# Kernel tuning notes

Hardware: AMD Instinct MI355X
Metric: run time of the kernel (lower is better)

The kernel has to match this reference:

```python
import jax, jax.numpy as jnp
import numpy as np

NH, WS, SS = 8, 7, 3  # num_heads, window_size, shift_size
EPS = 1e-5


def _rel_pos_index(ws):
    coords = np.stack(np.meshgrid(np.arange(ws), np.arange(ws), indexing='ij'))
    coords = coords.reshape(2, -1)                      # [2, L]
    rel = coords[:, :, None] - coords[:, None, :]       # [2, L, L]
    rel = rel.transpose(1, 2, 0) + (ws - 1)
    return rel[..., 0] * (2 * ws - 1) + rel[..., 1]     # [L, L] int


def _attn_mask(H, W, ws, ss):
    # region labels for shifted-window masking (torchvision semantics)
    img = np.zeros((H, W))
    slices = (slice(0, -ws), slice(-ws, -ss), slice(-ss, None))
    cnt = 0
    for hs in slices:
        for wsl in slices:
            img[hs, wsl] = cnt
            cnt += 1
    win = img.reshape(H // ws, ws, W // ws, ws).transpose(0, 2, 1, 3).reshape(-1, ws * ws)
    mask = (win[:, None, :] != win[:, :, None]).astype(np.float32) * (-100.0)
    return mask  # [nWin, L, L]


def _layernorm(x, gamma, beta):
    mu = jnp.mean(x, axis=-1, keepdims=True)
    var = jnp.mean(jnp.square(x - mu), axis=-1, keepdims=True)
    return (x - mu) * jax.lax.rsqrt(var + EPS) * gamma + beta


def _swin_attention(x, qkv_w, qkv_b, proj_w, proj_b, rpb_table):
    B, H, W, C = x.shape
    HD = C // NH
    L = WS * WS
    nH, nW = H // WS, W // WS
    # cyclic shift
    xs = jnp.roll(x, shift=(-SS, -SS), axis=(1, 2))
    # window partition -> [B*nWin, L, C]
    xw = xs.reshape(B, nH, WS, nW, WS, C).transpose(0, 1, 3, 2, 4, 5).reshape(B * nH * nW, L, C)
    qkv = jnp.einsum('nlc,dc->nld', xw, qkv_w) + qkv_b
    qkv = qkv.reshape(-1, L, 3, NH, HD).transpose(2, 0, 3, 1, 4)  # [3, N, h, L, d]
    q, k, v = qkv[0] * (HD ** -0.5), qkv[1], qkv[2]
    attn = jnp.einsum('nhid,nhjd->nhij', q, k)  # [N, h, L, L]
    bias = rpb_table[jnp.asarray(_rel_pos_index(WS))]  # [L, L, h]
    attn = attn + bias.transpose(2, 0, 1)[None]
    mask = jnp.asarray(_attn_mask(H, W, WS, SS))  # [nWin, L, L]
    nwin = nH * nW
    attn = attn.reshape(B, nwin, NH, L, L) + mask[None, :, None]
    attn = jax.nn.softmax(attn.reshape(-1, NH, L, L), axis=-1)
    out = jnp.einsum('nhij,nhjd->nhid', attn, v).transpose(0, 2, 1, 3).reshape(-1, L, C)
    out = jnp.einsum('nlc,dc->nld', out, proj_w) + proj_b
    # reverse windows and shift
    out = out.reshape(B, nH, nW, WS, WS, C).transpose(0, 1, 3, 2, 4, 5).reshape(B, H, W, C)
    return jnp.roll(out, shift=(SS, SS), axis=(1, 2))


def setup_inputs() -> dict:
    key = jax.random.key(0)
    ks = jax.random.split(key, 8)
    B, H, W, C = 32, 56, 56, 256
    F = 4 * C
    s = 0.02
    return {
        'x': jax.random.normal(ks[0], (B, H, W, C), jnp.float32),
        'qkv_w': jax.random.normal(ks[1], (3 * C, C), jnp.float32) * s,
        'qkv_b': jnp.zeros((3 * C,), jnp.float32),
        'proj_w': jax.random.normal(ks[2], (C, C), jnp.float32) * s,
        'proj_b': jnp.zeros((C,), jnp.float32),
        'rpb_table': jax.random.normal(ks[3], ((2 * WS - 1) ** 2, NH), jnp.float32) * s,
        'gamma1': jnp.ones((C,), jnp.float32),
        'beta1': jnp.zeros((C,), jnp.float32),
        'w1': jax.random.normal(ks[4], (C, F), jnp.float32) * s,
        'b1': jax.random.normal(ks[5], (F,), jnp.float32) * 1e-6,
        'w2': jax.random.normal(ks[6], (F, C), jnp.float32) * s,
        'b2': jax.random.normal(ks[7], (C,), jnp.float32) * 1e-6,
        'gamma2': jnp.ones((C,), jnp.float32),
        'beta2': jnp.zeros((C,), jnp.float32),
    }


def reference(x, qkv_w, qkv_b, proj_w, proj_b, rpb_table, gamma1, beta1, w1, b1, w2, b2, gamma2, beta2):
    # post-norm residual block: x + norm1(attn(x)); x + norm2(mlp(x))
    a = _swin_attention(x, qkv_w, qkv_b, proj_w, proj_b, rpb_table)
    x = x + _layernorm(a, gamma1, beta1)
    h = jax.nn.gelu(jnp.einsum('bhwc,cf->bhwf', x, w1) + b1, approximate=False)
    m = jnp.einsum('bhwf,fc->bhwc', h, w2) + b2
    x = x + _layernorm(m, gamma2, beta2)
    return x
```

## Files before the change

kernel.cpp:

```cpp
#include <hip/hip_runtime.h>
#include <hip/hip_bf16.h>


typedef unsigned short ushort_t;
typedef short bf16x8 __attribute__((ext_vector_type(8)));
typedef float f32x4 __attribute__((ext_vector_type(4)));

__device__ __forceinline__ float bf2f(unsigned short u) {
    union { unsigned int i; float f; } x; x.i = ((unsigned int)u) << 16; return x.f;
}
__device__ __forceinline__ unsigned short f2bf(float f) {
    union { float f; unsigned int i; } x; x.f = f;
    unsigned int r = x.i + 0x7fffu + ((x.i >> 16) & 1u);
    return (unsigned short)(r >> 16);
}
__device__ __forceinline__ bf16x8 pack8(float4 a, float4 b) {
    bf16x8 r;
    r[0] = (short)f2bf(a.x); r[1] = (short)f2bf(a.y);
    r[2] = (short)f2bf(a.z); r[3] = (short)f2bf(a.w);
    r[4] = (short)f2bf(b.x); r[5] = (short)f2bf(b.y);
    r[6] = (short)f2bf(b.z); r[7] = (short)f2bf(b.w);
    return r;
}
__device__ __forceinline__ void gl_lds16(const ushort_t* g, ushort_t* l) {
    __builtin_amdgcn_global_load_lds((const __attribute__((address_space(1))) void*)g,
                                     (__attribute__((address_space(3))) void*)l, 16, 0, 0);
}

__device__ __forceinline__ long swin_src_off(int m) {
    int n = m / 49, l = m - n * 49;
    int b = n >> 6, win = n & 63;
    int wh = win >> 3, ww = win & 7;
    int i = l / 7, j = l - i * 7;
    int hs = wh * 7 + i + 3; if (hs >= 56) hs -= 56;
    int ws = ww * 7 + j + 3; if (ws >= 56) ws -= 56;
    return ((long)(b * 56 + hs) * 56 + ws) * 256;
}

__global__ __launch_bounds__(256)
void xgather(const float* __restrict__ x, ushort_t* __restrict__ xg)
{
    int t = blockIdx.x * 256 + threadIdx.x;
    int row = t >> 5, ch = (t & 31) * 8;
    const float* src = x + swin_src_off(row) + ch;
    float4 a = *(const float4*)src, b = *(const float4*)(src + 4);
    *(bf16x8*)(xg + (long)row * 256 + ch) = pack8(a, b);
}

template<int SRCT>
__global__ __launch_bounds__(256)
void convW(const float* __restrict__ src, ushort_t* __restrict__ dst, int N, int kshift)
{
    int idx = blockIdx.x * 256 + threadIdx.x;
    int kk = idx & ((1 << kshift) - 1), nn = idx >> kshift;
    float v = SRCT ? src[(long)kk * N + nn] : src[idx];
    dst[idx] = f2bf(v);
}

template<int ACT>
__global__ __launch_bounds__(256)
void gemm128(const ushort_t* __restrict__ A, const ushort_t* __restrict__ W,
             const float* __restrict__ bias, ushort_t* __restrict__ C,
             int M, int N, int K)
{
    __shared__ ushort_t As[128 * 32];
    __shared__ ushort_t Bs[128 * 32];
    const int t = threadIdx.x, lane = t & 63, wave = t >> 6;
    const int row0 = blockIdx.x * 128, col0 = blockIdx.y * 128;
    const int wm = (wave >> 1) * 64, wn = (wave & 1) * 64;

    const ushort_t* ag0 = A + (long)(row0 + (t >> 2)) * K + (t & 3) * 8;
    const ushort_t* ag1 = A + (long)(row0 + 64 + (t >> 2)) * K + (t & 3) * 8;
    const ushort_t* bg0 = W + (long)(col0 + (t >> 2)) * K + (t & 3) * 8;
    const ushort_t* bg1 = W + (long)(col0 + 64 + (t >> 2)) * K + (t & 3) * 8;
    ushort_t* la0 = &As[t * 8];        ushort_t* la1 = &As[2048 + t * 8];
    ushort_t* lb0 = &Bs[t * 8];        ushort_t* lb1 = &Bs[2048 + t * 8];

    f32x4 acc[4][4] = {};
    for (int k0 = 0; k0 < K; k0 += 32) {
        __syncthreads();
        gl_lds16(ag0 + k0, la0);
        gl_lds16(ag1 + k0, la1);
        gl_lds16(bg0 + k0, lb0);
        gl_lds16(bg1 + k0, lb1);
        __syncthreads();
        bf16x8 af[4], bw[4];
        #pragma unroll
        for (int i = 0; i < 4; i++) {
            af[i] = *(const bf16x8*)&As[(wm + i * 16 + (lane & 15)) * 32 + (lane >> 4) * 8];
            bw[i] = *(const bf16x8*)&Bs[(wn + i * 16 + (lane & 15)) * 32 + (lane >> 4) * 8];
        }
        #pragma unroll
        for (int mi = 0; mi < 4; mi++)
            #pragma unroll
            for (int ni = 0; ni < 4; ni++)
                acc[mi][ni] = __builtin_amdgcn_mfma_f32_16x16x32_bf16(af[mi], bw[ni], acc[mi][ni], 0, 0, 0);
    }
    #pragma unroll
    for (int mi = 0; mi < 4; mi++)
        #pragma unroll
        for (int ni = 0; ni < 4; ni++) {
            const int c = col0 + wn + ni * 16 + (lane & 15);
            const float bv = bias[c];
            #pragma unroll
            for (int r = 0; r < 4; r++) {
                const int rr = row0 + wm + mi * 16 + (lane >> 4) * 4 + r;
                float v = acc[mi][ni][r] + bv;
                if (ACT) v = 0.5f * v * (1.0f + erff(v * 0.70710678118654752f));
                C[(long)rr * N + c] = f2bf(v);
            }
        }
}

__global__ __launch_bounds__(64)
void attn_mfma(const ushort_t* __restrict__ qkv, const float* __restrict__ rpb,
               ushort_t* __restrict__ out)
{
    __shared__ ushort_t v_t[32 * 72];
    __shared__ ushort_t p_lds[64 * 72];
    __shared__ float bias_s[169];

    const int blk = blockIdx.x;
    const int n = blk >> 3, h = blk & 7;
    const int l = threadIdx.x;
    const long wbase = (long)n * 49 * 768 + h * 32;
    const float scale = 0.17677669529663687f;

    {
        int j = min(l, 48);
        const ushort_t* vr = qkv + wbase + (long)j * 768 + 512;
        #pragma unroll
        for (int c = 0; c < 4; c++) {
            bf16x8 vv = *(const bf16x8*)(vr + c * 8);
            #pragma unroll
            for (int e = 0; e < 8; e++) v_t[(c * 8 + e) * 72 + l] = (ushort_t)vv[e];
        }
    }
    for (int idx = l; idx < 169; idx += 64) bias_s[idx] = rpb[idx * 8 + h];
    __syncthreads();

    f32x4 s[4][4] = {};
    {
        bf16x8 aq[4], bk[4];
        #pragma unroll
        for (int mt = 0; mt < 4; mt++) {
            int i = min(mt * 16 + (l & 15), 48);
            aq[mt] = *(const bf16x8*)(qkv + wbase + (long)i * 768 + (l >> 4) * 8);
        }
        #pragma unroll
        for (int nt = 0; nt < 4; nt++) {
            int j = min(nt * 16 + (l & 15), 48);
            bk[nt] = *(const bf16x8*)(qkv + wbase + (long)j * 768 + 256 + (l >> 4) * 8);
        }
        #pragma unroll
        for (int mt = 0; mt < 4; mt++)
            #pragma unroll
            for (int nt = 0; nt < 4; nt++)
                s[mt][nt] = __builtin_amdgcn_mfma_f32_16x16x32_bf16(aq[mt], bk[nt], s[mt][nt], 0, 0, 0);
    }

    const int win = n & 63, wh = win >> 3, ww = win & 7;
    int yj[4], xj[4], regj[4]; bool jv[4];
    #pragma unroll
    for (int nt = 0; nt < 4; nt++) {
        int j = nt * 16 + (l & 15);
        jv[nt] = (j <= 48);
        int jc = min(j, 48);
        yj[nt] = jc / 7; xj[nt] = jc - yj[nt] * 7;
        int hs = wh * 7 + yj[nt], wsx = ww * 7 + xj[nt];
        regj[nt] = (hs < 49 ? 0 : (hs < 53 ? 1 : 2)) * 3 + (wsx < 49 ? 0 : (wsx < 53 ? 1 : 2));
    }
    float rinv[4][4];
    #pragma unroll
    for (int mt = 0; mt < 4; mt++) {
        #pragma unroll
        for (int r = 0; r < 4; r++) {
            int i = mt * 16 + (l >> 4) * 4 + r;
            int ic = min(i, 48);
            int yi = ic / 7, xi = ic - yi * 7;
            int hs = wh * 7 + yi, wsx = ww * 7 + xi;
            int regi = (hs < 49 ? 0 : (hs < 53 ? 1 : 2)) * 3 + (wsx < 49 ? 0 : (wsx < 53 ? 1 : 2));
            float val[4];
            #pragma unroll
            for (int nt = 0; nt < 4; nt++) {
                float v = s[mt][nt][r] * scale + bias_s[(yi - yj[nt] + 6) * 13 + (xi - xj[nt] + 6)];
                if (regi != regj[nt]) v -= 100.f;
                val[nt] = jv[nt] ? v : -1e30f;
            }
            float mx = fmaxf(fmaxf(val[0], val[1]), fmaxf(val[2], val[3]));
            #pragma unroll
            for (int off = 1; off <= 8; off <<= 1) mx = fmaxf(mx, __shfl_xor(mx, off));
            float sum = 0.f;
            #pragma unroll
            for (int nt = 0; nt < 4; nt++) { val[nt] = __expf(val[nt] - mx); sum += val[nt]; }
            #pragma unroll
            for (int off = 1; off <= 8; off <<= 1) sum += __shfl_xor(sum, off);
            rinv[mt][r] = 1.0f / sum;
            #pragma unroll
            for (int nt = 0; nt < 4; nt++)
                p_lds[i * 72 + nt * 16 + (l & 15)] = f2bf(val[nt]);
        }
    }
    __syncthreads();

    f32x4 o[4][2] = {};
    #pragma unroll
    for (int ks = 0; ks < 2; ks++) {
        bf16x8 pa[4], vb[2];
        #pragma unroll
        for (int mt = 0; mt < 4; mt++)
            pa[mt] = *(const bf16x8*)&p_lds[(mt * 16 + (l & 15)) * 72 + ks * 32 + (l >> 4) * 8];
        #pragma unroll
        for (int nt = 0; nt < 2; nt++)
            vb[nt] = *(const bf16x8*)&v_t[(nt * 16 + (l & 15)) * 72 + ks * 32 + (l >> 4) * 8];
        #pragma unroll
        for (int mt = 0; mt < 4; mt++)
            #pragma unroll
            for (int nt = 0; nt < 2; nt++)
                o[mt][nt] = __builtin_amdgcn_mfma_f32_16x16x32_bf16(pa[mt], vb[nt], o[mt][nt], 0, 0, 0);
    }
    #pragma unroll
    for (int mt = 0; mt < 4; mt++)
        #pragma unroll
        for (int r = 0; r < 4; r++) {
            int i = mt * 16 + (l >> 4) * 4 + r;
            if (i < 49) {
                float rs = rinv[mt][r];
                #pragma unroll
                for (int nt = 0; nt < 2; nt++) {
                    int d = nt * 16 + (l & 15);
                    out[((long)n * 49 + i) * 256 + h * 32 + d] = f2bf(o[mt][nt][r] * rs);
                }
            }
        }
}

__global__ __launch_bounds__(256)
void ln1_kernel(const ushort_t* __restrict__ proj, const float* __restrict__ x,
                const float* __restrict__ gamma, const float* __restrict__ beta,
                float* __restrict__ x1f, ushort_t* __restrict__ x1b)
{
    const int wave = threadIdx.x >> 6, lane = threadIdx.x & 63;
    const int p = blockIdx.x * 4 + wave;
    const int b = p / 3136, rem = p - b * 3136;
    const int hh = rem / 56, wc = rem - hh * 56;
    int hs = hh + 53; if (hs >= 56) hs -= 56;
    int ws = wc + 53; if (ws >= 56) ws -= 56;
    const int wh = hs / 7, ii = hs - wh * 7;
    const int wwi = ws / 7, jj = ws - wwi * 7;
    const long srow = (long)(b * 64 + wh * 8 + wwi) * 49 + ii * 7 + jj;
    const int c = lane * 4;

    ushort4 av = *(const ushort4*)(proj + srow * 256 + c);
    float a0 = bf2f(av.x), a1 = bf2f(av.y), a2 = bf2f(av.z), a3 = bf2f(av.w);
    float s = a0 + a1 + a2 + a3;
    float ss = a0 * a0 + a1 * a1 + a2 * a2 + a3 * a3;
    #pragma unroll
    for (int off = 32; off; off >>= 1) { s += __shfl_xor(s, off); ss += __shfl_xor(ss, off); }
    const float mu = s * (1.0f / 256.0f);
    const float rstd = rsqrtf(ss * (1.0f / 256.0f) - mu * mu + 1e-5f);

    float4 gv = *(const float4*)(gamma + c);
    float4 bev = *(const float4*)(beta + c);
    float4 xv = *(const float4*)(x + (long)p * 256 + c);
    float o0 = xv.x + (a0 - mu) * rstd * gv.x + bev.x;
    float o1 = xv.y + (a1 - mu) * rstd * gv.y + bev.y;
    float o2 = xv.z + (a2 - mu) * rstd * gv.z + bev.z;
    float o3 = xv.w + (a3 - mu) * rstd * gv.w + bev.w;
    *(float4*)(x1f + (long)p * 256 + c) = make_float4(o0, o1, o2, o3);
    ushort4 ob; ob.x = f2bf(o0); ob.y = f2bf(o1); ob.z = f2bf(o2); ob.w = f2bf(o3);
    *(ushort4*)(x1b + (long)p * 256 + c) = ob;
}

__global__ __launch_bounds__(256)
void ln2_kernel(const ushort_t* __restrict__ m, const float* __restrict__ x1f,
                const float* __restrict__ gamma, const float* __restrict__ beta,
                float* __restrict__ out)
{
    const int wave = threadIdx.x >> 6, lane = threadIdx.x & 63;
    const int p = blockIdx.x * 4 + wave;
    const int c = lane * 4;

    ushort4 av = *(const ushort4*)(m + (long)p * 256 + c);
    float a0 = bf2f(av.x), a1 = bf2f(av.y), a2 = bf2f(av.z), a3 = bf2f(av.w);
    float s = a0 + a1 + a2 + a3;
    float ss = a0 * a0 + a1 * a1 + a2 * a2 + a3 * a3;
    #pragma unroll
    for (int off = 32; off; off >>= 1) { s += __shfl_xor(s, off); ss += __shfl_xor(ss, off); }
    const float mu = s * (1.0f / 256.0f);
    const float rstd = rsqrtf(ss * (1.0f / 256.0f) - mu * mu + 1e-5f);

    float4 gv = *(const float4*)(gamma + c);
    float4 bev = *(const float4*)(beta + c);
    float4 xv = *(const float4*)(x1f + (long)p * 256 + c);
    float4 ov;
    ov.x = xv.x + (a0 - mu) * rstd * gv.x + bev.x;
    ov.y = xv.y + (a1 - mu) * rstd * gv.y + bev.y;
    ov.z = xv.z + (a2 - mu) * rstd * gv.z + bev.z;
    ov.w = xv.w + (a3 - mu) * rstd * gv.w + bev.w;
    *(float4*)(out + (long)p * 256 + c) = ov;
}

extern "C" void kernel_launch(void* const* d_in, const int* in_sizes, int n_in,
                              void* d_out, int out_size, void* d_ws, size_t ws_size,
                              hipStream_t stream) {
    const float* x      = (const float*)d_in[0];
    const float* qkv_w  = (const float*)d_in[1];
    const float* qkv_b  = (const float*)d_in[2];
    const float* proj_w = (const float*)d_in[3];
    const float* proj_b = (const float*)d_in[4];
    const float* rpb    = (const float*)d_in[5];
    const float* gamma1 = (const float*)d_in[6];
    const float* beta1  = (const float*)d_in[7];
    const float* w1     = (const float*)d_in[8];
    const float* b1     = (const float*)d_in[9];
    const float* w2     = (const float*)d_in[10];
    const float* b2     = (const float*)d_in[11];
    const float* gamma2 = (const float*)d_in[12];
    const float* beta2  = (const float*)d_in[13];
    float* outf = (float*)d_out;

    char* ob = (char*)d_out;
    ushort_t* xg      = (ushort_t*)ob;
    ushort_t* attnout = (ushort_t*)(ob + 51380224ULL);
    ushort_t* projb   = (ushort_t*)ob;
    ushort_t* x1b     = (ushort_t*)(ob + 51380224ULL);

    char* ws = (char*)d_ws;
    ushort_t* qkvb  = (ushort_t*)ws;
    float*    x1f   = (float*)ws;
    ushort_t* hbuf  = (ushort_t*)(ws + 102760448ULL);
    ushort_t* mbuf  = (ushort_t*)(ws + 154140672ULL);
    ushort_t* wqkvb = (ushort_t*)(ws + 205520896ULL);
    ushort_t* wprojb= (ushort_t*)(ws + 205520896ULL + 393216ULL);
    ushort_t* w1t   = (ushort_t*)(ws + 205520896ULL + 524288ULL);
    ushort_t* w2t   = (ushort_t*)(ws + 205520896ULL + 1048576ULL);

    const int M = 100352, MC = 25088;
    dim3 blk(256);
    xgather<<<dim3(M / 8), blk, 0, stream>>>(x, xg);
    convW<0><<<dim3(768),  blk, 0, stream>>>(qkv_w,  wqkvb,  768,  8);
    convW<0><<<dim3(256),  blk, 0, stream>>>(proj_w, wprojb, 256,  8);
    convW<1><<<dim3(1024), blk, 0, stream>>>(w1,     w1t,    1024, 8);
    convW<1><<<dim3(1024), blk, 0, stream>>>(w2,     w2t,    256, 10);
    gemm128<0><<<dim3(784, 6), blk, 0, stream>>>(xg, wqkvb, qkv_b, qkvb, M, 768, 256);
    attn_mfma<<<dim3(16384), dim3(64), 0, stream>>>(qkvb, rpb, attnout);
    gemm128<0><<<dim3(784, 2), blk, 0, stream>>>(attnout, wprojb, proj_b, projb, M, 256, 256);
    ln1_kernel<<<dim3(M / 4), blk, 0, stream>>>(projb, x, gamma1, beta1, x1f, x1b);
    for (int c4 = 0; c4 < 4; c4++) {
        const ushort_t* xc = x1b + (long)c4 * MC * 256;
        gemm128<1><<<dim3(196, 8), blk, 0, stream>>>(xc, w1t, b1, hbuf, MC, 1024, 256);
        gemm128<0><<<dim3(196, 2), blk, 0, stream>>>(hbuf, w2t, b2, mbuf + (long)c4 * MC * 256, MC, 256, 1024);
    }
    ln2_kernel<<<dim3(M / 4), blk, 0, stream>>>(mbuf, x1f, gamma2, beta2, outf);
}
```

Before: 602.7 us.

## Fuse proj GEMM with LN1 and whole MLP with LN2 into two kernels

Replaces the proj GEMM plus separate LN1 kernel with a single kernel computing a 128x256 output tile and doing the row LayerNorm, residual add and un-shift scatter in its epilogue. Replaces the chunked fc1/GELU/fc2 GEMMs and LN2 with one kernel that keeps a 128-row block's fc2 accumulators in registers, streams 32-wide hidden chunks through LDS and never writes the hidden activation to global memory. This removes large intermediate round trips and several launches. In exchange the MLP kernel uses many registers, syncs twice per chunk, and the proj epilogue writes scattered rows with uncoalesced scalar stores.

```diff
diff --git a/kernel.cpp b/kernel.cpp
--- a/kernel.cpp
+++ b/kernel.cpp
@@ -43,8 +43,7 @@
     int t = blockIdx.x * 256 + threadIdx.x;
     int row = t >> 5, ch = (t & 31) * 8;
     const float* src = x + swin_src_off(row) + ch;
-    float4 a = *(const float4*)src, b = *(const float4*)(src + 4);
-    *(bf16x8*)(xg + (long)row * 256 + ch) = pack8(a, b);
+    *(bf16x8*)(xg + (long)row * 256 + ch) = pack8(*(const float4*)src, *(const float4*)(src + 4));
 }
 
 template<int SRCT>
@@ -235,70 +234,177 @@
         }
 }
 
-__global__ __launch_bounds__(256)
-void ln1_kernel(const ushort_t* __restrict__ proj, const float* __restrict__ x,
-                const float* __restrict__ gamma, const float* __restrict__ beta,
-                float* __restrict__ x1f, ushort_t* __restrict__ x1b)
-{
-    const int wave = threadIdx.x >> 6, lane = threadIdx.x & 63;
-    const int p = blockIdx.x * 4 + wave;
-    const int b = p / 3136, rem = p - b * 3136;
-    const int hh = rem / 56, wc = rem - hh * 56;
-    int hs = hh + 53; if (hs >= 56) hs -= 56;
-    int ws = wc + 53; if (ws >= 56) ws -= 56;
-    const int wh = hs / 7, ii = hs - wh * 7;
-    const int wwi = ws / 7, jj = ws - wwi * 7;
-    const long srow = (long)(b * 64 + wh * 8 + wwi) * 49 + ii * 7 + jj;
-    const int c = lane * 4;
-
-    ushort4 av = *(const ushort4*)(proj + srow * 256 + c);
-    float a0 = bf2f(av.x), a1 = bf2f(av.y), a2 = bf2f(av.z), a3 = bf2f(av.w);
-    float s = a0 + a1 + a2 + a3;
-    float ss = a0 * a0 + a1 * a1 + a2 * a2 + a3 * a3;
-    #pragma unroll
-    for (int off = 32; off; off >>= 1) { s += __shfl_xor(s, off); ss += __shfl_xor(ss, off); }
-    const float mu = s * (1.0f / 256.0f);
-    const float rstd = rsqrtf(ss * (1.0f / 256.0f) - mu * mu + 1e-5f);
-
-    float4 gv = *(const float4*)(gamma + c);
-    float4 bev = *(const float4*)(beta + c);
-    float4 xv = *(const float4*)(x + (long)p * 256 + c);
-    float o0 = xv.x + (a0 - mu) * rstd * gv.x + bev.x;
-    float o1 = xv.y + (a1 - mu) * rstd * gv.y + bev.y;
-    float o2 = xv.z + (a2 - mu) * rstd * gv.z + bev.z;
-    float o3 = xv.w + (a3 - mu) * rstd * gv.w + bev.w;
-    *(float4*)(x1f + (long)p * 256 + c) = make_float4(o0, o1, o2, o3);
-    ushort4 ob; ob.x = f2bf(o0); ob.y = f2bf(o1); ob.z = f2bf(o2); ob.w = f2bf(o3);
-    *(ushort4*)(x1b + (long)p * 256 + c) = ob;
-}
-
-__global__ __launch_bounds__(256)
-void ln2_kernel(const ushort_t* __restrict__ m, const float* __restrict__ x1f,
-                const float* __restrict__ gamma, const float* __restrict__ beta,
-                float* __restrict__ out)
-{
-    const int wave = threadIdx.x >> 6, lane = threadIdx.x & 63;
-    const int p = blockIdx.x * 4 + wave;
-    const int c = lane * 4;
-
-    ushort4 av = *(const ushort4*)(m + (long)p * 256 + c);
-    float a0 = bf2f(av.x), a1 = bf2f(av.y), a2 = bf2f(av.z), a3 = bf2f(av.w);
-    float s = a0 + a1 + a2 + a3;
-    float ss = a0 * a0 + a1 * a1 + a2 * a2 + a3 * a3;
-    #pragma unroll
-    for (int off = 32; off; off >>= 1) { s += __shfl_xor(s, off); ss += __shfl_xor(ss, off); }
-    const float mu = s * (1.0f / 256.0f);
-    const float rstd = rsqrtf(ss * (1.0f / 256.0f) - mu * mu + 1e-5f);
-
-    float4 gv = *(const float4*)(gamma + c);
-    float4 bev = *(const float4*)(beta + c);
-    float4 xv = *(const float4*)(x1f + (long)p * 256 + c);
-    float4 ov;
-    ov.x = xv.x + (a0 - mu) * rstd * gv.x + bev.x;
-    ov.y = xv.y + (a1 - mu) * rstd * gv.y + bev.y;
-    ov.z = xv.z + (a2 - mu) * rstd * gv.z + bev.z;
-    ov.w = xv.w + (a3 - mu) * rstd * gv.w + bev.w;
-    *(float4*)(out + (long)p * 256 + c) = ov;
+__global__ __launch_bounds__(512)
+void projln1(const ushort_t* __restrict__ A, const ushort_t* __restrict__ W,
+             const float* __restrict__ pb, const float* __restrict__ x,
+             const float* __restrict__ gamma, const float* __restrict__ beta,
+             float* __restrict__ x1f, ushort_t* __restrict__ x1b)
+{
+    __shared__ ushort_t As[128 * 32];
+    __shared__ ushort_t Bs[256 * 32];
+    __shared__ float red_s[128][4];
+    __shared__ float red_ss[128][4];
+    __shared__ int srow_s[128];
+    const int t = threadIdx.x, lane = t & 63, w = t >> 6;
+    const int row0 = blockIdx.x * 128;
+    const int wm = (w >> 2) * 64, wn = (w & 3) * 64;
+
+    if (t < 128) srow_s[t] = (int)(swin_src_off(row0 + t) >> 8);
+
+    const ushort_t* ag = A + (long)(row0 + (t >> 2)) * 256 + (t & 3) * 8;
+    f32x4 acc[4][4] = {};
+    for (int k0 = 0; k0 < 256; k0 += 32) {
+        __syncthreads();
+        gl_lds16(ag + k0, &As[t * 8]);
+        #pragma unroll
+        for (int i = 0; i < 2; i++) {
+            int u = i * 512 + t;
+            gl_lds16(W + (long)(u >> 2) * 256 + k0 + (u & 3) * 8, &Bs[u * 8]);
+        }
+        __syncthreads();
+        bf16x8 af[4], bw[4];
+        #pragma unroll
+        for (int i2 = 0; i2 < 4; i2++) {
+            af[i2] = *(const bf16x8*)&As[(wm + i2 * 16 + (lane & 15)) * 32 + (lane >> 4) * 8];
+            bw[i2] = *(const bf16x8*)&Bs[(wn + i2 * 16 + (lane & 15)) * 32 + (lane >> 4) * 8];
+        }
+        #pragma unroll
+        for (int mi = 0; mi < 4; mi++)
+            #pragma unroll
+            for (int ni = 0; ni < 4; ni++)
+                acc[mi][ni] = __builtin_amdgcn_mfma_f32_16x16x32_bf16(af[mi], bw[ni], acc[mi][ni], 0, 0, 0);
+    }
+    float pbv[4], g1v[4], be1v[4];
+    #pragma unroll
+    for (int ni = 0; ni < 4; ni++) {
+        int col = wn + ni * 16 + (lane & 15);
+        pbv[ni] = pb[col]; g1v[ni] = gamma[col]; be1v[ni] = beta[col];
+    }
+    #pragma unroll
+    for (int mi = 0; mi < 4; mi++)
+        #pragma unroll
+        for (int rr = 0; rr < 4; rr++) {
+            float s = 0.f, ss = 0.f;
+            #pragma unroll
+            for (int ni = 0; ni < 4; ni++) {
+                float v = acc[mi][ni][rr] + pbv[ni];
+                acc[mi][ni][rr] = v; s += v; ss += v * v;
+            }
+            #pragma unroll
+            for (int off = 1; off <= 8; off <<= 1) { s += __shfl_xor(s, off); ss += __shfl_xor(ss, off); }
+            if ((lane & 15) == 0) {
+                int r = wm + mi * 16 + (lane >> 4) * 4 + rr;
+                red_s[r][w & 3] = s; red_ss[r][w & 3] = ss;
+            }
+        }
+    __syncthreads();
+    #pragma unroll
+    for (int mi = 0; mi < 4; mi++)
+        #pragma unroll
+        for (int rr = 0; rr < 4; rr++) {
+            const int r = wm + mi * 16 + (lane >> 4) * 4 + rr;
+            const float s = red_s[r][0] + red_s[r][1] + red_s[r][2] + red_s[r][3];
+            const float ss = red_ss[r][0] + red_ss[r][1] + red_ss[r][2] + red_ss[r][3];
+            const float mu = s * (1.0f / 256.0f);
+            const float rstd = rsqrtf(ss * (1.0f / 256.0f) - mu * mu + 1e-5f);
+            const long sp = srow_s[r];
+            #pragma unroll
+            for (int ni = 0; ni < 4; ni++) {
+                int col = wn + ni * 16 + (lane & 15);
+                float o = x[sp * 256 + col] + (acc[mi][ni][rr] - mu) * rstd * g1v[ni] + be1v[ni];
+                x1f[sp * 256 + col] = o;
+                x1b[sp * 256 + col] = f2bf(o);
+            }
+        }
+}
+
+__global__ __launch_bounds__(512)
+void mlp_fused(const ushort_t* __restrict__ x1b, const float* __restrict__ x1f,
+               const ushort_t* __restrict__ w1t, const ushort_t* __restrict__ w2t,
+               const float* __restrict__ b1, const float* __restrict__ b2,
+               const float* __restrict__ gamma, const float* __restrict__ beta,
+               float* __restrict__ out)
+{
+    __shared__ ushort_t W1c[32 * 256];
+    __shared__ ushort_t W2c[256 * 32];
+    __shared__ ushort_t hbuf[8 * 16 * 40];
+    const int t = threadIdx.x, lane = t & 63, w = t >> 6;
+    const long row0 = (long)blockIdx.x * 128;
+    const int rbase = w * 16;
+
+    bf16x8 xa[8];
+    const ushort_t* xrow = x1b + (row0 + rbase + (lane & 15)) * 256 + (lane >> 4) * 8;
+    #pragma unroll
+    for (int ks = 0; ks < 8; ks++) xa[ks] = *(const bf16x8*)(xrow + ks * 32);
+
+    f32x4 accm[16] = {};
+    for (int hc = 0; hc < 32; hc++) {
+        __syncthreads();
+        #pragma unroll
+        for (int i = 0; i < 2; i++) {
+            int u = i * 512 + t;
+            int r1 = u >> 5, c1 = (u & 31) ^ (r1 & 7);
+            gl_lds16(w1t + ((hc * 32 + r1) << 8) + c1 * 8, &W1c[u * 8]);
+            int n2 = u >> 2, c2 = (u & 3) ^ (n2 & 3);
+            gl_lds16(w2t + ((long)n2 << 10) + hc * 32 + c2 * 8, &W2c[u * 8]);
+        }
+        __syncthreads();
+        f32x4 acch[2] = {};
+        #pragma unroll
+        for (int ks = 0; ks < 8; ks++) {
+            #pragma unroll
+            for (int nt = 0; nt < 2; nt++) {
+                int hid = nt * 16 + (lane & 15);
+                int su = ((ks << 2) | (lane >> 4)) ^ (hid & 7);
+                bf16x8 bw = *(const bf16x8*)&W1c[(hid << 8) + (su << 3)];
+                acch[nt] = __builtin_amdgcn_mfma_f32_16x16x32_bf16(xa[ks], bw, acch[nt], 0, 0, 0);
+            }
+        }
+        #pragma unroll
+        for (int nt = 0; nt < 2; nt++) {
+            int hid = nt * 16 + (lane & 15);
+            float bv = b1[hc * 32 + hid];
+            #pragma unroll
+            for (int r = 0; r < 4; r++) {
+                float v = acch[nt][r] + bv;
+                v = 0.5f * v * (1.0f + erff(v * 0.70710678118654752f));
+                hbuf[w * 640 + ((lane >> 4) * 4 + r) * 40 + hid] = f2bf(v);
+            }
+        }
+        bf16x8 pa = *(const bf16x8*)&hbuf[w * 640 + (lane & 15) * 40 + (lane >> 4) * 8];
+        #pragma unroll
+        for (int nt = 0; nt < 16; nt++) {
+            int n = nt * 16 + (lane & 15);
+            int su = (lane >> 4) ^ (n & 3);
+            bf16x8 bw = *(const bf16x8*)&W2c[(n << 5) + (su << 3)];
+            accm[nt] = __builtin_amdgcn_mfma_f32_16x16x32_bf16(pa, bw, accm[nt], 0, 0, 0);
+        }
+    }
+    float b2v[16], g2v[16], be2v[16];
+    #pragma unroll
+    for (int nt = 0; nt < 16; nt++) {
+        int col = nt * 16 + (lane & 15);
+        b2v[nt] = b2[col]; g2v[nt] = gamma[col]; be2v[nt] = beta[col];
+    }
+    #pragma unroll
+    for (int rr = 0; rr < 4; rr++) {
+        const long grow = row0 + rbase + (lane >> 4) * 4 + rr;
+        float s = 0.f, ss = 0.f, mv[16];
+        #pragma unroll
+        for (int nt = 0; nt < 16; nt++) {
+            float v = accm[nt][rr] + b2v[nt];
+            mv[nt] = v; s += v; ss += v * v;
+        }
+        #pragma unroll
+        for (int off = 1; off <= 8; off <<= 1) { s += __shfl_xor(s, off); ss += __shfl_xor(ss, off); }
+        const float mu = s * (1.0f / 256.0f);
+        const float rstd = rsqrtf(ss * (1.0f / 256.0f) - mu * mu + 1e-5f);
+        #pragma unroll
+        for (int nt = 0; nt < 16; nt++) {
+            int col = nt * 16 + (lane & 15);
+            out[grow * 256 + col] = x1f[grow * 256 + col] + (mv[nt] - mu) * rstd * g2v[nt] + be2v[nt];
+        }
+    }
 }
 
 extern "C" void kernel_launch(void* const* d_in, const int* in_sizes, int n_in,
@@ -323,20 +429,17 @@
     char* ob = (char*)d_out;
     ushort_t* xg      = (ushort_t*)ob;
     ushort_t* attnout = (ushort_t*)(ob + 51380224ULL);
-    ushort_t* projb   = (ushort_t*)ob;
-    ushort_t* x1b     = (ushort_t*)(ob + 51380224ULL);
 
     char* ws = (char*)d_ws;
     ushort_t* qkvb  = (ushort_t*)ws;
     float*    x1f   = (float*)ws;
-    ushort_t* hbuf  = (ushort_t*)(ws + 102760448ULL);
-    ushort_t* mbuf  = (ushort_t*)(ws + 154140672ULL);
+    ushort_t* x1b   = (ushort_t*)(ws + 102760448ULL);
     ushort_t* wqkvb = (ushort_t*)(ws + 205520896ULL);
-    ushort_t* wprojb= (ushort_t*)(ws + 205520896ULL + 393216ULL);
-    ushort_t* w1t   = (ushort_t*)(ws + 205520896ULL + 524288ULL);
-    ushort_t* w2t   = (ushort_t*)(ws + 205520896ULL + 1048576ULL);
-
-    const int M = 100352, MC = 25088;
+    ushort_t* wprojb= (ushort_t*)(ws + 205914112ULL);
+    ushort_t* w1t   = (ushort_t*)(ws + 206045184ULL);
+    ushort_t* w2t   = (ushort_t*)(ws + 206569472ULL);
+
+    const int M = 100352;
     dim3 blk(256);
     xgather<<<dim3(M / 8), blk, 0, stream>>>(x, xg);
     convW<0><<<dim3(768),  blk, 0, stream>>>(qkv_w,  wqkvb,  768,  8);
@@ -345,12 +448,8 @@
     convW<1><<<dim3(1024), blk, 0, stream>>>(w2,     w2t,    256, 10);
     gemm128<0><<<dim3(784, 6), blk, 0, stream>>>(xg, wqkvb, qkv_b, qkvb, M, 768, 256);
     attn_mfma<<<dim3(16384), dim3(64), 0, stream>>>(qkvb, rpb, attnout);
-    gemm128<0><<<dim3(784, 2), blk, 0, stream>>>(attnout, wprojb, proj_b, projb, M, 256, 256);
-    ln1_kernel<<<dim3(M / 4), blk, 0, stream>>>(projb, x, gamma1, beta1, x1f, x1b);
-    for (int c4 = 0; c4 < 4; c4++) {
-        const ushort_t* xc = x1b + (long)c4 * MC * 256;
-        gemm128<1><<<dim3(196, 8), blk, 0, stream>>>(xc, w1t, b1, hbuf, MC, 1024, 256);
-        gemm128<0><<<dim3(196, 2), blk, 0, stream>>>(hbuf, w2t, b2, mbuf + (long)c4 * MC * 256, MC, 256, 1024);
-    }
-    ln2_kernel<<<dim3(M / 4), blk, 0, stream>>>(mbuf, x1f, gamma2, beta2, outf);
-}
+    projln1<<<dim3(784), dim3(512), 0, stream>>>(attnout, wprojb, proj_b, x,
+                                                 gamma1, beta1, x1f, x1b);
+    mlp_fused<<<dim3(784), dim3(512), 0, stream>>>(x1b, x1f, w1t, w2t, b1, b2,
+                                                   gamma2, beta2, outf);
+}
```

Result: slower. 646.3 us (+7.2%).
